# Optimization experiments

Measured on AMD Instinct MI355X. Metric: run time of the kernel, lower is better.

The kernel has to match this reference:

```python
import jax, jax.numpy as jnp
from jax import lax
import numpy as np

K = 3
PAD = (K - 1) // 2
EPS = 1e-5


def setup_inputs() -> dict:
    key = jax.random.key(0)
    k0, k1, k2, k3 = jax.random.split(key, 4)
    B, C, O, H, W = 8, 128, 128, 64, 64
    x = jax.random.normal(k0, (B, C, H, W), jnp.float32)
    bn_gamma = jnp.ones((C,), jnp.float32)
    bn_beta = jnp.zeros((C,), jnp.float32)
    bn_mean = jnp.zeros((C,), jnp.float32)
    bn_var = jnp.ones((C,), jnp.float32)
    # small offset-conv weights -> realistic sub-pixel offsets
    w_off = jax.random.normal(k1, (2 * K * K, C, K, K), jnp.float32) * 0.01
    b_off = jnp.zeros((2 * K * K,), jnp.float32)
    w_dconv = jax.random.normal(k2, (O, C, K, K), jnp.float32) * (1.0 / np.sqrt(C * K * K))
    b_dconv = jax.random.normal(k3, (O,), jnp.float32) * 0.01
    return dict(x=x, bn_gamma=bn_gamma, bn_beta=bn_beta, bn_mean=bn_mean,
                bn_var=bn_var, w_off=w_off, b_off=b_off,
                w_dconv=w_dconv, b_dconv=b_dconv)


def _conv2d(x, w, b):
    y = lax.conv_general_dilated(
        x, w, window_strides=(1, 1), padding=[(PAD, PAD), (PAD, PAD)],
        dimension_numbers=('NCHW', 'OIHW', 'NCHW'))
    return y + b[None, :, None, None]


def _deform_conv2d(x, offsets, w, b):
    # torchvision DeformConv2d semantics (deform_groups=1, groups=1, stride=1)
    B, C, H, W = x.shape
    KK = K * K
    off = offsets.reshape(B, KK, 2, H, W)  # (dy, dx) per kernel tap
    dy, dx = off[:, :, 0], off[:, :, 1]    # [B,KK,H,W]
    kh = (jnp.arange(KK) // K).astype(x.dtype)
    kw = (jnp.arange(KK) % K).astype(x.dtype)
    # sampling positions: p0 + pk - pad + offset
    py = dy + jnp.arange(H, dtype=x.dtype)[None, None, :, None] + (kh - PAD)[None, :, None, None]
    px = dx + jnp.arange(W, dtype=x.dtype)[None, None, None, :] + (kw - PAD)[None, :, None, None]
    y0 = jnp.floor(py)
    x0 = jnp.floor(px)
    wy = py - y0
    wx = px - x0
    y0i = y0.astype(jnp.int32)
    x0i = x0.astype(jnp.int32)
    xflat = x.reshape(B, C, H * W)

    def gather(yi, xi):
        valid = (yi >= 0) & (yi < H) & (xi >= 0) & (xi < W)
        idx = jnp.clip(yi, 0, H - 1) * W + jnp.clip(xi, 0, W - 1)  # [B,KK,H,W]
        vals = jax.vmap(lambda xf, ii: xf[:, ii])(xflat, idx)      # [B,C,KK,H,W]
        return vals * valid[:, None].astype(x.dtype)

    # bilinear sample with implicit zero padding outside the image
    v = (((1 - wy) * (1 - wx))[:, None] * gather(y0i, x0i)
         + ((1 - wy) * wx)[:, None] * gather(y0i, x0i + 1)
         + (wy * (1 - wx))[:, None] * gather(y0i + 1, x0i)
         + (wy * wx)[:, None] * gather(y0i + 1, x0i + 1))  # [B,C,KK,H,W]
    out = jnp.einsum('bckhw,ock->bohw', v, w.reshape(w.shape[0], C, KK))
    return out + b[None, :, None, None]


def reference(x, bn_gamma, bn_beta, bn_mean, bn_var, w_off, b_off, w_dconv, b_dconv):
    # BN (inference form) + ReLU
    inv = bn_gamma * lax.rsqrt(bn_var + EPS)
    h = jnp.maximum((x - bn_mean[None, :, None, None]) * inv[None, :, None, None]
                    + bn_beta[None, :, None, None], 0.0)
    offsets = _conv2d(h, w_off, b_off)          # [B, 2*K*K, H, W]
    return _deform_conv2d(h, offsets, w_dconv, b_dconv)
```

## Files before the change

kernel.cpp:

```cpp
#include <hip/hip_runtime.h>

#define CC 128
#define OO 128
#define HH 64
#define WW 64
#define HW (HH*WW)

typedef __attribute__((ext_vector_type(8))) __bf16 bf16x8;
typedef __attribute__((ext_vector_type(4))) __bf16 bf16x4;
typedef __attribute__((ext_vector_type(4))) float  f32x4;

__global__ __launch_bounds__(256) void prep(
    const float* __restrict__ x,
    const float* __restrict__ gamma, const float* __restrict__ beta,
    const float* __restrict__ mean,  const float* __restrict__ var,
    const float* __restrict__ w_dconv, const float* __restrict__ w_off,
    __bf16* __restrict__ h,
    __bf16* __restrict__ wt_swz,
    __bf16* __restrict__ woff_swz)
{
    __shared__ float inv_s[128], bb_s[128];
    __shared__ __bf16 tile[64 * 130];
    int blk = blockIdx.x;
    int tid = threadIdx.x;

    if (blk >= 512) {
        int idx = (blk - 512) * 256 + tid;
        if (idx < 147456) {
            int j    = idx & 7;
            int lane = (idx >> 3) & 63;
            int og   = (idx >> 9) & 7;
            int ks   = (idx >> 12) & 3;
            int kk   = idx >> 14;
            int o = og * 16 + (lane & 15);
            int c = ks * 32 + (lane >> 4) * 8 + j;
            wt_swz[idx] = (__bf16)w_dconv[(o * 128 + c) * 9 + kk];
        }
        if (idx < 36864) {
            int j    = idx & 7;
            int lane = (idx >> 3) & 63;
            int og   = (idx >> 9) & 1;
            int ks   = (idx >> 10) & 3;
            int kk   = idx >> 12;
            int o = og * 16 + (lane & 15);
            int c = ks * 32 + (lane >> 4) * 8 + j;
            float v = (o < 18) ? w_off[o * 1152 + c * 9 + kk] : 0.f;
            woff_swz[idx] = (__bf16)v;
        }
        return;
    }

    int b = blk & 7, y = blk >> 3;
    if (tid < 128) {
        float iv = gamma[tid] * rsqrtf(var[tid] + 1e-5f);
        inv_s[tid] = iv;
        bb_s[tid]  = beta[tid] - mean[tid] * iv;
    }
    __syncthreads();

    const float* xb = x + (size_t)b * CC * HW + (size_t)y * WW;
    #pragma unroll
    for (int i = 0; i < 8; ++i) {
        int idx = i * 256 + tid;
        int c = idx >> 4, x4 = idx & 15;
        float4 v = *(const float4*)(xb + (size_t)c * HW + x4 * 4);
        float iv = inv_s[c], bb = bb_s[c];
        tile[(x4 * 4 + 0) * 130 + c] = (__bf16)fmaxf(v.x * iv + bb, 0.f);
        tile[(x4 * 4 + 1) * 130 + c] = (__bf16)fmaxf(v.y * iv + bb, 0.f);
        tile[(x4 * 4 + 2) * 130 + c] = (__bf16)fmaxf(v.z * iv + bb, 0.f);
        tile[(x4 * 4 + 3) * 130 + c] = (__bf16)fmaxf(v.w * iv + bb, 0.f);
    }
    __syncthreads();

    __bf16* hb = h + ((size_t)b * HW + (size_t)y * WW) * CC;
    #pragma unroll
    for (int i = 0; i < 2; ++i) {
        int idx = i * 256 + tid;
        int xx = idx >> 3, c16 = idx & 7;
        const uint* src = (const uint*)&tile[xx * 130 + c16 * 16];
        uint r0 = src[0], r1 = src[1], r2 = src[2], r3 = src[3];
        uint r4 = src[4], r5 = src[5], r6 = src[6], r7 = src[7];
        uint* dst = (uint*)(hb + (size_t)xx * CC + c16 * 16);
        *(uint4*)dst       = (uint4){r0, r1, r2, r3};
        *(uint4*)(dst + 4) = (uint4){r4, r5, r6, r7};
    }
}

__global__ __launch_bounds__(256) void offset_mfma(
    const __bf16* __restrict__ h,
    const __bf16* __restrict__ woff_swz,
    const float* __restrict__ b_off,
    float* __restrict__ offs)
{
    __shared__ __align__(16) __bf16 at[2][64 * 136];
    int blk = blockIdx.x;
    int b = blk & 7, y = blk >> 3;
    int tid = threadIdx.x;
    int lane = tid & 63;
    int wv  = __builtin_amdgcn_readfirstlane(tid >> 6);
    int l15 = lane & 15, quad = lane >> 4;

    const __bf16* hb = h + (size_t)b * HW * CC;
    const bf16x8* w8 = (const bf16x8*)woff_swz;

    int sxx = tid >> 4, sc8 = tid & 15;

    f32x4 acc[2];
    acc[0] = (f32x4){0.f, 0.f, 0.f, 0.f};
    acc[1] = (f32x4){0.f, 0.f, 0.f, 0.f};

    uint4 pa[4];
    {
        int yy = y - 1;
        bool yok = (yy >= 0);
        #pragma unroll
        for (int i = 0; i < 4; ++i) {
            int idx = i * 256 + tid;
            int xx = idx >> 4, c8 = idx & 15;
            int xs = xx - 1;
            pa[i] = (uint4){0u, 0u, 0u, 0u};
            if (yok && xs >= 0)
                pa[i] = *(const uint4*)(hb + ((size_t)yy * WW + xs) * CC + c8 * 8);
        }
    }

    for (int kk = 0; kk < 9; ++kk) {
        int buf = kk & 1;
        #pragma unroll
        for (int i = 0; i < 4; ++i) {
            int idx = i * 256 + tid;
            int xx = idx >> 4, c8 = idx & 15;
            *(uint4*)&at[buf][xx * 136 + c8 * 8] = pa[i];
        }
        if (kk < 8) {
            int k2 = kk + 1;
            int dy = k2 / 3 - 1, dx = k2 % 3 - 1;
            int yy = y + dy;
            bool yok = (yy >= 0) && (yy < HH);
            #pragma unroll
            for (int i = 0; i < 4; ++i) {
                int idx = i * 256 + tid;
                int xx = idx >> 4, c8 = idx & 15;
                int xs = xx + dx;
                pa[i] = (uint4){0u, 0u, 0u, 0u};
                if (yok && xs >= 0 && xs < WW)
                    pa[i] = *(const uint4*)(hb + ((size_t)yy * WW + xs) * CC + c8 * 8);
            }
        }
        asm volatile("s_waitcnt lgkmcnt(0)" ::: "memory");
        __builtin_amdgcn_s_barrier();
        #pragma unroll
        for (int ks = 0; ks < 4; ++ks) {
            int kb = ks * 32 + quad * 8;
            bf16x8 a  = *(const bf16x8*)&at[buf][(wv * 16 + l15) * 136 + kb];
            bf16x8 b0 = w8[((kk * 4 + ks) * 2 + 0) * 64 + lane];
            bf16x8 b1 = w8[((kk * 4 + ks) * 2 + 1) * 64 + lane];
            acc[0] = __builtin_amdgcn_mfma_f32_16x16x32_bf16(a, b0, acc[0], 0, 0, 0);
            acc[1] = __builtin_amdgcn_mfma_f32_16x16x32_bf16(a, b1, acc[1], 0, 0, 0);
        }
    }

    size_t ob = (size_t)b * 18 * HW + (size_t)y * WW;
    #pragma unroll
    for (int nt = 0; nt < 2; ++nt) {
        int oc = nt * 16 + l15;
        if (oc < 18) {
            float bias = b_off[oc];
            #pragma unroll
            for (int r = 0; r < 4; ++r) {
                int xx = wv * 16 + quad * 4 + r;
                offs[ob + (size_t)oc * HW + xx] = acc[nt][r] + bias;
            }
        }
    }
}

__global__ __launch_bounds__(256, 2) void deform_conv_mfma(
    const __bf16* __restrict__ h,
    const float* __restrict__ offs,
    const __bf16* __restrict__ wt_swz,
    const float* __restrict__ b_dconv,
    float* __restrict__ out)
{
    __shared__ float pw[576 * 4];
    __shared__ int   pidx[576 * 4];
    __shared__ __align__(16) __bf16 vt[2][64 * 136];

    int blk = blockIdx.x;
    int b = blk & 7, y = blk >> 3;
    int tid = threadIdx.x;

    const __bf16* hb = h + (size_t)b * HW * CC;
    size_t offbase = (size_t)b * 18 * HW + (size_t)y * WW;

    for (int e = tid; e < 576; e += 256) {
        int kk = e >> 6, xx = e & 63;
        float dy = offs[offbase + (size_t)(2 * kk) * HW + xx];
        float dx = offs[offbase + (size_t)(2 * kk + 1) * HW + xx];
        float py = dy + (float)y + (float)(kk / 3 - 1);
        float px = dx + (float)xx + (float)(kk % 3 - 1);
        float fy = floorf(py), fx = floorf(px);
        int y0 = (int)fy, x0 = (int)fx;
        float wy = py - fy, wx = px - fx;
        int y1 = y0 + 1, x1 = x0 + 1;
        bool vy0 = (y0 >= 0) && (y0 < HH);
        bool vy1 = (y1 >= 0) && (y1 < HH);
        bool vx0 = (x0 >= 0) && (x0 < WW);
        bool vx1 = (x1 >= 0) && (x1 < WW);
        int yc0 = min(max(y0, 0), HH - 1), yc1 = min(max(y1, 0), HH - 1);
        int xc0 = min(max(x0, 0), WW - 1), xc1 = min(max(x1, 0), WW - 1);
        pw[e * 4 + 0] = (vy0 && vx0) ? (1.f - wy) * (1.f - wx) : 0.f;
        pw[e * 4 + 1] = (vy0 && vx1) ? (1.f - wy) * wx         : 0.f;
        pw[e * 4 + 2] = (vy1 && vx0) ? wy * (1.f - wx)         : 0.f;
        pw[e * 4 + 3] = (vy1 && vx1) ? wy * wx                 : 0.f;
        pidx[e * 4 + 0] = (yc0 * WW + xc0) * CC;
        pidx[e * 4 + 1] = (yc0 * WW + xc1) * CC;
        pidx[e * 4 + 2] = (yc1 * WW + xc0) * CC;
        pidx[e * 4 + 3] = (yc1 * WW + xc1) * CC;
    }
    __syncthreads();

    int lane = tid & 63;
    int wv   = __builtin_amdgcn_readfirstlane(tid >> 6);
    int l15  = lane & 15, quad = lane >> 4;
    const bf16x8* w8 = (const bf16x8*)wt_swz;

    f32x4 acc[4][2];
    #pragma unroll
    for (int mt = 0; mt < 4; ++mt)
        #pragma unroll
        for (int nt = 0; nt < 2; ++nt)
            acc[mt][nt] = (f32x4){0.f, 0.f, 0.f, 0.f};

    bf16x8 pt0[4], pt1[4], pt2[4], pt3[4];
    #pragma unroll
    for (int i = 0; i < 4; ++i) {
        int idx = i * 256 + tid;
        int xx = idx >> 4, c8 = idx & 15;
        int e = xx;
        pt0[i] = *(const bf16x8*)(hb + pidx[e * 4 + 0] + c8 * 8);
        pt1[i] = *(const bf16x8*)(hb + pidx[e * 4 + 1] + c8 * 8);
        pt2[i] = *(const bf16x8*)(hb + pidx[e * 4 + 2] + c8 * 8);
        pt3[i] = *(const bf16x8*)(hb + pidx[e * 4 + 3] + c8 * 8);
    }

    for (int kk = 0; kk < 9; ++kk) {
        int buf = kk & 1;
        #pragma unroll
        for (int i = 0; i < 4; ++i) {
            int idx = i * 256 + tid;
            int xx = idx >> 4, c8 = idx & 15;
            int e = (kk << 6) + xx;
            float w0 = pw[e * 4 + 0], w1 = pw[e * 4 + 1];
            float w2 = pw[e * 4 + 2], w3 = pw[e * 4 + 3];
            bf16x8 pk;
            #pragma unroll
            for (int q = 0; q < 8; ++q) {
                float v = w0 * (float)pt0[i][q] + w1 * (float)pt1[i][q]
                        + w2 * (float)pt2[i][q] + w3 * (float)pt3[i][q];
                pk[q] = (__bf16)v;
            }
            *(bf16x8*)&vt[buf][xx * 136 + c8 * 8] = pk;
        }
        if (kk < 8) {
            #pragma unroll
            for (int i = 0; i < 4; ++i) {
                int idx = i * 256 + tid;
                int xx = idx >> 4, c8 = idx & 15;
                int e2 = ((kk + 1) << 6) + xx;
                pt0[i] = *(const bf16x8*)(hb + pidx[e2 * 4 + 0] + c8 * 8);
                pt1[i] = *(const bf16x8*)(hb + pidx[e2 * 4 + 1] + c8 * 8);
                pt2[i] = *(const bf16x8*)(hb + pidx[e2 * 4 + 2] + c8 * 8);
                pt3[i] = *(const bf16x8*)(hb + pidx[e2 * 4 + 3] + c8 * 8);
            }
        }
        asm volatile("s_waitcnt lgkmcnt(0)" ::: "memory");
        __builtin_amdgcn_s_barrier();
        #pragma unroll
        for (int ks = 0; ks < 4; ++ks) {
            int kb = ks * 32 + quad * 8;
            bf16x8 b0 = w8[((kk * 4 + ks) * 8 + 2 * wv + 0) * 64 + lane];
            bf16x8 b1 = w8[((kk * 4 + ks) * 8 + 2 * wv + 1) * 64 + lane];
            bf16x8 a0 = *(const bf16x8*)&vt[buf][(0 * 16 + l15) * 136 + kb];
            bf16x8 a1 = *(const bf16x8*)&vt[buf][(1 * 16 + l15) * 136 + kb];
            bf16x8 a2 = *(const bf16x8*)&vt[buf][(2 * 16 + l15) * 136 + kb];
            bf16x8 a3 = *(const bf16x8*)&vt[buf][(3 * 16 + l15) * 136 + kb];
            acc[0][0] = __builtin_amdgcn_mfma_f32_16x16x32_bf16(a0, b0, acc[0][0], 0, 0, 0);
            acc[1][0] = __builtin_amdgcn_mfma_f32_16x16x32_bf16(a1, b0, acc[1][0], 0, 0, 0);
            acc[2][0] = __builtin_amdgcn_mfma_f32_16x16x32_bf16(a2, b0, acc[2][0], 0, 0, 0);
            acc[3][0] = __builtin_amdgcn_mfma_f32_16x16x32_bf16(a3, b0, acc[3][0], 0, 0, 0);
            acc[0][1] = __builtin_amdgcn_mfma_f32_16x16x32_bf16(a0, b1, acc[0][1], 0, 0, 0);
            acc[1][1] = __builtin_amdgcn_mfma_f32_16x16x32_bf16(a1, b1, acc[1][1], 0, 0, 0);
            acc[2][1] = __builtin_amdgcn_mfma_f32_16x16x32_bf16(a2, b1, acc[2][1], 0, 0, 0);
            acc[3][1] = __builtin_amdgcn_mfma_f32_16x16x32_bf16(a3, b1, acc[3][1], 0, 0, 0);
        }
    }

    size_t ob = (size_t)b * OO * HW + (size_t)y * WW;
    #pragma unroll
    for (int nt = 0; nt < 2; ++nt) {
        int o = wv * 32 + nt * 16 + l15;
        float bias = b_dconv[o];
        #pragma unroll
        for (int mt = 0; mt < 4; ++mt) {
            int xb = mt * 16 + quad * 4;
            float4 r;
            r.x = acc[mt][nt][0] + bias;
            r.y = acc[mt][nt][1] + bias;
            r.z = acc[mt][nt][2] + bias;
            r.w = acc[mt][nt][3] + bias;
            *(float4*)&out[ob + (size_t)o * HW + xb] = r;
        }
    }
}

extern "C" void kernel_launch(void* const* d_in, const int* in_sizes, int n_in,
                              void* d_out, int out_size, void* d_ws, size_t ws_size,
                              hipStream_t stream)
{
    const float* x       = (const float*)d_in[0];
    const float* gamma   = (const float*)d_in[1];
    const float* beta    = (const float*)d_in[2];
    const float* mean    = (const float*)d_in[3];
    const float* var     = (const float*)d_in[4];
    const float* w_off   = (const float*)d_in[5];
    const float* b_off   = (const float*)d_in[6];
    const float* w_dconv = (const float*)d_in[7];
    const float* b_dconv = (const float*)d_in[8];
    float* out = (float*)d_out;

    char* ws = (char*)d_ws;
    __bf16* h_bf     = (__bf16*)ws;
    float*  offs     = (float*)(ws + 8388608);
    __bf16* wt_swz   = (__bf16*)(ws + 10747904);
    __bf16* woff_swz = (__bf16*)(ws + 11042816);

    prep<<<1232, 256, 0, stream>>>(x, gamma, beta, mean, var,
                                   w_dconv, w_off, h_bf, wt_swz, woff_swz);
    offset_mfma<<<512, 256, 0, stream>>>(h_bf, woff_swz, b_off, offs);
    deform_conv_mfma<<<512, 256, 0, stream>>>(h_bf, offs, wt_swz, b_dconv, out);
}
```

Before: 125.6 us.

## Fuse offset convolution into deformable conv kernel via shared-memory offsets

Merges the offset-conv MFMA kernel into the deformable-conv kernel. Each block computes its row's 18 offset channels, keeps them in LDS, and reuses the vt buffer as staging. This removes one kernel launch and the global write and read of the offsets tensor. In exchange each block runs both phases in sequence, which adds LDS use and register pressure under the 2-block occupancy bound.

```diff
diff --git a/kernel.cpp b/kernel.cpp
--- a/kernel.cpp
+++ b/kernel.cpp
@@ -86,98 +86,10 @@
     }
 }
 
-__global__ __launch_bounds__(256) void offset_mfma(
+__global__ __launch_bounds__(256, 2) void fused_mfma(
     const __bf16* __restrict__ h,
     const __bf16* __restrict__ woff_swz,
     const float* __restrict__ b_off,
-    float* __restrict__ offs)
-{
-    __shared__ __align__(16) __bf16 at[2][64 * 136];
-    int blk = blockIdx.x;
-    int b = blk & 7, y = blk >> 3;
-    int tid = threadIdx.x;
-    int lane = tid & 63;
-    int wv  = __builtin_amdgcn_readfirstlane(tid >> 6);
-    int l15 = lane & 15, quad = lane >> 4;
-
-    const __bf16* hb = h + (size_t)b * HW * CC;
-    const bf16x8* w8 = (const bf16x8*)woff_swz;
-
-    int sxx = tid >> 4, sc8 = tid & 15;
-
-    f32x4 acc[2];
-    acc[0] = (f32x4){0.f, 0.f, 0.f, 0.f};
-    acc[1] = (f32x4){0.f, 0.f, 0.f, 0.f};
-
-    uint4 pa[4];
-    {
-        int yy = y - 1;
-        bool yok = (yy >= 0);
-        #pragma unroll
-        for (int i = 0; i < 4; ++i) {
-            int idx = i * 256 + tid;
-            int xx = idx >> 4, c8 = idx & 15;
-            int xs = xx - 1;
-            pa[i] = (uint4){0u, 0u, 0u, 0u};
-            if (yok && xs >= 0)
-                pa[i] = *(const uint4*)(hb + ((size_t)yy * WW + xs) * CC + c8 * 8);
-        }
-    }
-
-    for (int kk = 0; kk < 9; ++kk) {
-        int buf = kk & 1;
-        #pragma unroll
-        for (int i = 0; i < 4; ++i) {
-            int idx = i * 256 + tid;
-            int xx = idx >> 4, c8 = idx & 15;
-            *(uint4*)&at[buf][xx * 136 + c8 * 8] = pa[i];
-        }
-        if (kk < 8) {
-            int k2 = kk + 1;
-            int dy = k2 / 3 - 1, dx = k2 % 3 - 1;
-            int yy = y + dy;
-            bool yok = (yy >= 0) && (yy < HH);
-            #pragma unroll
-            for (int i = 0; i < 4; ++i) {
-                int idx = i * 256 + tid;
-                int xx = idx >> 4, c8 = idx & 15;
-                int xs = xx + dx;
-                pa[i] = (uint4){0u, 0u, 0u, 0u};
-                if (yok && xs >= 0 && xs < WW)
-                    pa[i] = *(const uint4*)(hb + ((size_t)yy * WW + xs) * CC + c8 * 8);
-            }
-        }
-        asm volatile("s_waitcnt lgkmcnt(0)" ::: "memory");
-        __builtin_amdgcn_s_barrier();
-        #pragma unroll
-        for (int ks = 0; ks < 4; ++ks) {
-            int kb = ks * 32 + quad * 8;
-            bf16x8 a  = *(const bf16x8*)&at[buf][(wv * 16 + l15) * 136 + kb];
-            bf16x8 b0 = w8[((kk * 4 + ks) * 2 + 0) * 64 + lane];
-            bf16x8 b1 = w8[((kk * 4 + ks) * 2 + 1) * 64 + lane];
-            acc[0] = __builtin_amdgcn_mfma_f32_16x16x32_bf16(a, b0, acc[0], 0, 0, 0);
-            acc[1] = __builtin_amdgcn_mfma_f32_16x16x32_bf16(a, b1, acc[1], 0, 0, 0);
-        }
-    }
-
-    size_t ob = (size_t)b * 18 * HW + (size_t)y * WW;
-    #pragma unroll
-    for (int nt = 0; nt < 2; ++nt) {
-        int oc = nt * 16 + l15;
-        if (oc < 18) {
-            float bias = b_off[oc];
-            #pragma unroll
-            for (int r = 0; r < 4; ++r) {
-                int xx = wv * 16 + quad * 4 + r;
-                offs[ob + (size_t)oc * HW + xx] = acc[nt][r] + bias;
-            }
-        }
-    }
-}
-
-__global__ __launch_bounds__(256, 2) void deform_conv_mfma(
-    const __bf16* __restrict__ h,
-    const float* __restrict__ offs,
     const __bf16* __restrict__ wt_swz,
     const float* __restrict__ b_dconv,
     float* __restrict__ out)
@@ -185,18 +97,94 @@
     __shared__ float pw[576 * 4];
     __shared__ int   pidx[576 * 4];
     __shared__ __align__(16) __bf16 vt[2][64 * 136];
+    __shared__ float offs_lds[18 * 64];
 
     int blk = blockIdx.x;
     int b = blk & 7, y = blk >> 3;
     int tid = threadIdx.x;
+    int lane = tid & 63;
+    int wv  = __builtin_amdgcn_readfirstlane(tid >> 6);
+    int l15 = lane & 15, quad = lane >> 4;
 
     const __bf16* hb = h + (size_t)b * HW * CC;
-    size_t offbase = (size_t)b * 18 * HW + (size_t)y * WW;
+
+    {
+        const bf16x8* w8 = (const bf16x8*)woff_swz;
+
+        f32x4 acc[2];
+        acc[0] = (f32x4){0.f, 0.f, 0.f, 0.f};
+        acc[1] = (f32x4){0.f, 0.f, 0.f, 0.f};
+
+        uint4 pa[4];
+        {
+            int yy = y - 1;
+            bool yok = (yy >= 0);
+            #pragma unroll
+            for (int i = 0; i < 4; ++i) {
+                int idx = i * 256 + tid;
+                int xx = idx >> 4, c8 = idx & 15;
+                int xs = xx - 1;
+                pa[i] = (uint4){0u, 0u, 0u, 0u};
+                if (yok && xs >= 0)
+                    pa[i] = *(const uint4*)(hb + ((size_t)yy * WW + xs) * CC + c8 * 8);
+            }
+        }
+
+        for (int kk = 0; kk < 9; ++kk) {
+            int buf = kk & 1;
+            #pragma unroll
+            for (int i = 0; i < 4; ++i) {
+                int idx = i * 256 + tid;
+                int xx = idx >> 4, c8 = idx & 15;
+                *(uint4*)&vt[buf][xx * 136 + c8 * 8] = pa[i];
+            }
+            if (kk < 8) {
+                int k2 = kk + 1;
+                int dy = k2 / 3 - 1, dx = k2 % 3 - 1;
+                int yy = y + dy;
+                bool yok = (yy >= 0) && (yy < HH);
+                #pragma unroll
+                for (int i = 0; i < 4; ++i) {
+                    int idx = i * 256 + tid;
+                    int xx = idx >> 4, c8 = idx & 15;
+                    int xs = xx + dx;
+                    pa[i] = (uint4){0u, 0u, 0u, 0u};
+                    if (yok && xs >= 0 && xs < WW)
+                        pa[i] = *(const uint4*)(hb + ((size_t)yy * WW + xs) * CC + c8 * 8);
+                }
+            }
+            asm volatile("s_waitcnt lgkmcnt(0)" ::: "memory");
+            __builtin_amdgcn_s_barrier();
+            #pragma unroll
+            for (int ks = 0; ks < 4; ++ks) {
+                int kb = ks * 32 + quad * 8;
+                bf16x8 a  = *(const bf16x8*)&vt[buf][(wv * 16 + l15) * 136 + kb];
+                bf16x8 b0 = w8[((kk * 4 + ks) * 2 + 0) * 64 + lane];
+                bf16x8 b1 = w8[((kk * 4 + ks) * 2 + 1) * 64 + lane];
+                acc[0] = __builtin_amdgcn_mfma_f32_16x16x32_bf16(a, b0, acc[0], 0, 0, 0);
+                acc[1] = __builtin_amdgcn_mfma_f32_16x16x32_bf16(a, b1, acc[1], 0, 0, 0);
+            }
+        }
+
+        #pragma unroll
+        for (int nt = 0; nt < 2; ++nt) {
+            int oc = nt * 16 + l15;
+            if (oc < 18) {
+                float bias = b_off[oc];
+                #pragma unroll
+                for (int r = 0; r < 4; ++r) {
+                    int xx = wv * 16 + quad * 4 + r;
+                    offs_lds[oc * 64 + xx] = acc[nt][r] + bias;
+                }
+            }
+        }
+    }
+    __syncthreads();
 
     for (int e = tid; e < 576; e += 256) {
         int kk = e >> 6, xx = e & 63;
-        float dy = offs[offbase + (size_t)(2 * kk) * HW + xx];
-        float dx = offs[offbase + (size_t)(2 * kk + 1) * HW + xx];
+        float dy = offs_lds[(2 * kk) * 64 + xx];
+        float dx = offs_lds[(2 * kk + 1) * 64 + xx];
         float py = dy + (float)y + (float)(kk / 3 - 1);
         float px = dx + (float)xx + (float)(kk % 3 - 1);
         float fy = floorf(py), fx = floorf(px);
@@ -220,9 +208,6 @@
     }
     __syncthreads();
 
-    int lane = tid & 63;
-    int wv   = __builtin_amdgcn_readfirstlane(tid >> 6);
-    int l15  = lane & 15, quad = lane >> 4;
     const bf16x8* w8 = (const bf16x8*)wt_swz;
 
     f32x4 acc[4][2];
@@ -331,12 +316,11 @@
 
     char* ws = (char*)d_ws;
     __bf16* h_bf     = (__bf16*)ws;
-    float*  offs     = (float*)(ws + 8388608);
-    __bf16* wt_swz   = (__bf16*)(ws + 10747904);
-    __bf16* woff_swz = (__bf16*)(ws + 11042816);
+    __bf16* wt_swz   = (__bf16*)(ws + 8388608);
+    __bf16* woff_swz = (__bf16*)(ws + 8683520);
 
     prep<<<1232, 256, 0, stream>>>(x, gamma, beta, mean, var,
                                    w_dconv, w_off, h_bf, wt_swz, woff_swz);
-    offset_mfma<<<512, 256, 0, stream>>>(h_bf, woff_swz, b_off, offs);
-    deform_conv_mfma<<<512, 256, 0, stream>>>(h_bf, offs, wt_swz, b_dconv, out);
+    fused_mfma<<<512, 256, 0, stream>>>(h_bf, woff_swz, b_off,
+                                        wt_swz, b_dconv, out);
 }
```

Measured after the change: 123.1 us. 1.02x faster.
